# Optimization experiments

Hardware: AMD Instinct MI355X
Metric: run time of the kernel (lower is better)

## Reference

```python
import jax, jax.numpy as jnp
import numpy as np

P, R, S = 512, 128, 128   # num_proposal, ref_length, src_length
K = 3                      # top-k per row/column
THRESHOLD = 0.05
MUTUAL = False
CONDITIONAL = True


def setup_inputs() -> dict:
    key = jax.random.key(0)
    k1, k2, k3, k4 = jax.random.split(key, 4)
    return {
        "matching_score_map": jax.random.normal(k1, (P, R, S), dtype=jnp.float32),
        "ref_knn_masks": jax.random.bernoulli(k2, 0.9, (P, R)),
        "src_knn_masks": jax.random.bernoulli(k3, 0.9, (P, S)),
        "node_corr_scores": jax.random.uniform(k4, (P,), dtype=jnp.float32),
    }


def reference(matching_score_map, ref_knn_masks, src_knn_masks, node_corr_scores):
    # matching_score_map: [P, R, S] log-scores -> exp, as in torch forward
    m = jnp.exp(matching_score_map)
    p, r, s = m.shape
    # corr_mask_map = ref_mask[:, :, None] & src_mask[:, None, :] -> [P, R, S]
    corr_mask_map = jnp.logical_and(ref_knn_masks[:, :, None], src_knn_masks[:, None, :])

    pidx = jnp.arange(p)[:, None, None]

    # top-k along src dim (dim=2), scatter back into a sparse score map
    ref_topk_scores, ref_topk_idx = jax.lax.top_k(m, K)           # [P, R, K]
    ridx = jnp.arange(r)[None, :, None]
    ref_score_map = jnp.zeros_like(m).at[pidx, ridx, ref_topk_idx].set(ref_topk_scores)

    # top-k along ref dim (dim=1): transpose, top_k, scatter, transpose back
    mt = jnp.swapaxes(m, 1, 2)                                    # [P, S, R]
    src_topk_scores, src_topk_idx = jax.lax.top_k(mt, K)          # [P, S, K]
    sidx = jnp.arange(s)[None, :, None]
    src_score_map = jnp.swapaxes(
        jnp.zeros_like(mt).at[pidx, sidx, src_topk_idx].set(src_topk_scores), 1, 2
    )

    ref_corr_map = jnp.logical_and(ref_score_map > THRESHOLD, corr_mask_map)
    src_corr_map = jnp.logical_and(src_score_map > THRESHOLD, corr_mask_map)

    score_map = (ref_score_map + src_score_map) * 0.5
    if MUTUAL:
        corr_map = jnp.logical_and(ref_corr_map, src_corr_map)
    else:
        corr_map = jnp.logical_or(ref_corr_map, src_corr_map)
    if CONDITIONAL:
        score_map = score_map * node_corr_scores[:, None, None]
    return score_map, corr_map
```

## Files before the change

### kernel.cpp

```cpp
#include <hip/hip_runtime.h>


constexpr int NP = 512;
constexpr int NR = 128;
constexpr int NS = 128;
constexpr int RS = NR * NS;
constexpr float THRESHOLD = 0.05f;
constexpr float NEG_INF = -3.4e38f;

__device__ __forceinline__ void top3_insert(float v, float& m0, float& m1, float& m2) {
    bool g2 = v > m2, g1 = v > m1, g0 = v > m0;
    float n2 = g1 ? m1 : (g2 ? v : m2);
    float n1 = g0 ? m0 : (g1 ? v : m1);
    float n0 = g0 ? v : m0;
    m0 = n0; m1 = n1; m2 = n2;
}

__device__ __forceinline__ void shfl_merge3(int d, float& m0, float& m1, float& m2) {
    float o0 = __shfl_xor(m0, d);
    float o1 = __shfl_xor(m1, d);
    float o2 = __shfl_xor(m2, d);
    top3_insert(o0, m0, m1, m2);
    top3_insert(o1, m0, m1, m2);
    top3_insert(o2, m0, m1, m2);
}

__global__ __launch_bounds__(512, 4) void fused_kernel(
    const float* __restrict__ in,
    const int*   __restrict__ rmask,
    const int*   __restrict__ smask,
    const float* __restrict__ ncs,
    float*       __restrict__ ws,
    float*       __restrict__ out)
{
    __shared__ float tile[RS];
    const int p = blockIdx.x;
    const int t = threadIdx.x;

    const float4* b4 = (const float4*)(in + (size_t)p * RS);
    float4*       t4 = (float4*)tile;

    #pragma unroll
    for (int k = 0; k < 8; ++k) {
        int i4 = t + k * 512;
        t4[i4] = b4[i4];
    }
    __syncthreads();

    float* ws_row = ws + (size_t)p * 256;
    float* ws_col = ws_row + 128;

    {
        const int row = t >> 2, q = t & 3;
        const int base4 = row * 32 + q * 8;
        float m0 = NEG_INF, m1 = NEG_INF, m2 = NEG_INF;
        #pragma unroll
        for (int j = 0; j < 8; ++j) {
            int jj = (j + t) & 7;
            float4 v = t4[base4 + jj];
            top3_insert(v.x, m0, m1, m2);
            top3_insert(v.y, m0, m1, m2);
            top3_insert(v.z, m0, m1, m2);
            top3_insert(v.w, m0, m1, m2);
        }
        shfl_merge3(1, m0, m1, m2);
        shfl_merge3(2, m0, m1, m2);
        if (q == 0) ws_row[row] = m2;
    }

    {
        const int col = t >> 2, seg = t & 3;
        float m0 = NEG_INF, m1 = NEG_INF, m2 = NEG_INF;
        #pragma unroll 8
        for (int i = 0; i < 32; ++i) {
            float v = tile[(seg * 32 + i) * NS + col];
            top3_insert(v, m0, m1, m2);
        }
        shfl_merge3(1, m0, m1, m2);
        shfl_merge3(2, m0, m1, m2);
        if (seg == 0) ws_col[col] = m2;
    }

    __threadfence_block();
    __syncthreads();

    const float  nc = ncs[p];
    const float4 tc = ((const float4*)ws_col)[t & 31];
    const int4   ms = ((const int4*)(smask + (size_t)p * NS))[t & 31];
    float trow[8];
    int   mrow[8];
    #pragma unroll
    for (int k = 0; k < 8; ++k) {
        int row = (t >> 5) + k * 16;
        trow[k] = ws_row[row];
        mrow[k] = rmask[p * NR + row];
    }

    float4* sc4 = (float4*)(out + (size_t)p * RS);
    float4* co4 = (float4*)(out + (size_t)(NP + p) * RS);
    #pragma unroll
    for (int k = 0; k < 8; ++k) {
        int C = t + k * 512;
        float4 x = t4[C];
        float tr = trow[k];
        bool  mr = mrow[k] != 0;
        float4 sc, co;

        {   float m  = __expf(x.x);
            float rs = (x.x >= tr)   ? m : 0.f;
            float cs = (x.x >= tc.x) ? m : 0.f;
            sc.x = 0.5f * (rs + cs) * nc;
            co.x = (mr && (ms.x != 0) && (rs > THRESHOLD || cs > THRESHOLD)) ? 1.f : 0.f; }
        {   float m  = __expf(x.y);
            float rs = (x.y >= tr)   ? m : 0.f;
            float cs = (x.y >= tc.y) ? m : 0.f;
            sc.y = 0.5f * (rs + cs) * nc;
            co.y = (mr && (ms.y != 0) && (rs > THRESHOLD || cs > THRESHOLD)) ? 1.f : 0.f; }
        {   float m  = __expf(x.z);
            float rs = (x.z >= tr)   ? m : 0.f;
            float cs = (x.z >= tc.z) ? m : 0.f;
            sc.z = 0.5f * (rs + cs) * nc;
            co.z = (mr && (ms.z != 0) && (rs > THRESHOLD || cs > THRESHOLD)) ? 1.f : 0.f; }
        {   float m  = __expf(x.w);
            float rs = (x.w >= tr)   ? m : 0.f;
            float cs = (x.w >= tc.w) ? m : 0.f;
            sc.w = 0.5f * (rs + cs) * nc;
            co.w = (mr && (ms.w != 0) && (rs > THRESHOLD || cs > THRESHOLD)) ? 1.f : 0.f; }

        sc4[C] = sc;
        co4[C] = co;
    }
}

extern "C" void kernel_launch(void* const* d_in, const int* in_sizes, int n_in,
                              void* d_out, int out_size, void* d_ws, size_t ws_size,
                              hipStream_t stream) {
    const float* msm   = (const float*)d_in[0];
    const int*   rmask = (const int*)  d_in[1];
    const int*   smask = (const int*)  d_in[2];
    const float* ncs   = (const float*)d_in[3];
    float* out = (float*)d_out;
    float* ws  = (float*)d_ws;

    fused_kernel<<<NP, 512, 0, stream>>>(msm, rmask, smask, ncs, ws, out);
}
```

Baseline: 98.16 us.

## Fuse row top-k into global load and XOR-swizzle shared tile

The row top-3 is now computed in registers while the tile is loaded from global memory, so the separate shared-memory row pass and the ws_row round trip are gone. The shared tile is stored with an XOR swizzle on float4 columns, meant to reduce bank conflicts on the strided column reads. The output pass is remapped so each thread handles its own row, keeping the row threshold and mask in registers. In exchange, global loads are no longer contiguous across threads (stride-32 float4 per row group), which may hurt load and store coalescing, and per-iteration loads of column thresholds and src masks are added.

```diff
diff --git a/kernel.cpp b/kernel.cpp
--- a/kernel.cpp
+++ b/kernel.cpp
@@ -33,77 +33,62 @@
     float*       __restrict__ ws,
     float*       __restrict__ out)
 {
-    __shared__ float tile[RS];
-    const int p = blockIdx.x;
-    const int t = threadIdx.x;
+    __shared__ float4 tile4[RS / 4];
+    const int p   = blockIdx.x;
+    const int t   = threadIdx.x;
+    const int row = t >> 2;
+    const int q   = t & 3;
 
     const float4* b4 = (const float4*)(in + (size_t)p * RS);
-    float4*       t4 = (float4*)tile;
+    float* ws_col = ws + (size_t)p * 128;
 
+    float r0 = NEG_INF, r1 = NEG_INF, r2 = NEG_INF;
     #pragma unroll
-    for (int k = 0; k < 8; ++k) {
-        int i4 = t + k * 512;
-        t4[i4] = b4[i4];
+    for (int j = 0; j < 8; ++j) {
+        int c4 = q + 4 * j;
+        float4 v = b4[row * 32 + c4];
+        tile4[row * 32 + (c4 ^ (row & 31))] = v;
+        top3_insert(v.x, r0, r1, r2);
+        top3_insert(v.y, r0, r1, r2);
+        top3_insert(v.z, r0, r1, r2);
+        top3_insert(v.w, r0, r1, r2);
     }
+    shfl_merge3(1, r0, r1, r2);
+    shfl_merge3(2, r0, r1, r2);
+    const float tr = r2;
     __syncthreads();
-
-    float* ws_row = ws + (size_t)p * 256;
-    float* ws_col = ws_row + 128;
-
-    {
-        const int row = t >> 2, q = t & 3;
-        const int base4 = row * 32 + q * 8;
-        float m0 = NEG_INF, m1 = NEG_INF, m2 = NEG_INF;
-        #pragma unroll
-        for (int j = 0; j < 8; ++j) {
-            int jj = (j + t) & 7;
-            float4 v = t4[base4 + jj];
-            top3_insert(v.x, m0, m1, m2);
-            top3_insert(v.y, m0, m1, m2);
-            top3_insert(v.z, m0, m1, m2);
-            top3_insert(v.w, m0, m1, m2);
-        }
-        shfl_merge3(1, m0, m1, m2);
-        shfl_merge3(2, m0, m1, m2);
-        if (q == 0) ws_row[row] = m2;
-    }
 
     {
         const int col = t >> 2, seg = t & 3;
-        float m0 = NEG_INF, m1 = NEG_INF, m2 = NEG_INF;
+        const int c4c = col >> 2, cw = col & 3;
+        const float* tf = (const float*)tile4;
+        float c0 = NEG_INF, c1 = NEG_INF, c2 = NEG_INF;
         #pragma unroll 8
         for (int i = 0; i < 32; ++i) {
-            float v = tile[(seg * 32 + i) * NS + col];
-            top3_insert(v, m0, m1, m2);
+            int r = 4 * seg + (i & 3) + 16 * (i >> 2);
+            float v = tf[r * 128 + ((c4c ^ (r & 31)) << 2) + cw];
+            top3_insert(v, c0, c1, c2);
         }
-        shfl_merge3(1, m0, m1, m2);
-        shfl_merge3(2, m0, m1, m2);
-        if (seg == 0) ws_col[col] = m2;
+        shfl_merge3(1, c0, c1, c2);
+        shfl_merge3(2, c0, c1, c2);
+        if (seg == 0) ws_col[col] = c2;
     }
-
     __threadfence_block();
     __syncthreads();
 
-    const float  nc = ncs[p];
-    const float4 tc = ((const float4*)ws_col)[t & 31];
-    const int4   ms = ((const int4*)(smask + (size_t)p * NS))[t & 31];
-    float trow[8];
-    int   mrow[8];
-    #pragma unroll
-    for (int k = 0; k < 8; ++k) {
-        int row = (t >> 5) + k * 16;
-        trow[k] = ws_row[row];
-        mrow[k] = rmask[p * NR + row];
-    }
-
+    const float nc = ncs[p];
+    const bool  mr = rmask[p * NR + row] != 0;
     float4* sc4 = (float4*)(out + (size_t)p * RS);
     float4* co4 = (float4*)(out + (size_t)(NP + p) * RS);
+    const float4* wc4 = (const float4*)ws_col;
+    const int4*   sm4 = (const int4*)(smask + (size_t)p * NS);
+
     #pragma unroll
-    for (int k = 0; k < 8; ++k) {
-        int C = t + k * 512;
-        float4 x = t4[C];
-        float tr = trow[k];
-        bool  mr = mrow[k] != 0;
+    for (int j = 0; j < 8; ++j) {
+        int c4 = q + 4 * j;
+        float4 x  = tile4[row * 32 + (c4 ^ (row & 31))];
+        float4 tc = wc4[c4];
+        int4   ms = sm4[c4];
         float4 sc, co;
 
         {   float m  = __expf(x.x);
@@ -127,8 +112,8 @@
             sc.w = 0.5f * (rs + cs) * nc;
             co.w = (mr && (ms.w != 0) && (rs > THRESHOLD || cs > THRESHOLD)) ? 1.f : 0.f; }
 
-        sc4[C] = sc;
-        co4[C] = co;
+        sc4[row * 32 + c4] = sc;
+        co4[row * 32 + c4] = co;
     }
 }
 
```

Result: no change. 98.13 us (-0.0%).
